# Kernel optimization log

Hardware: AMD Instinct MI355X
Metric: run time of the kernel (lower is better)

## Reference

```python
import jax, jax.numpy as jnp
import numpy as np

N = 50000
E = 800000
DIM = 256
H = 8
HD = DIM // H


def setup_inputs() -> dict:
    key = jax.random.key(0)
    ks = jax.random.split(key, 8)
    s = 0.02
    return {
        "x": jax.random.normal(ks[0], (N, DIM), jnp.float32),
        "src": jax.random.randint(ks[1], (E,), 0, N, jnp.int32),
        "dst": jax.random.randint(ks[2], (E,), 0, N, jnp.int32),
        "Wqkv": jax.random.normal(ks[3], (DIM, 3 * DIM), jnp.float32) * s,
        "bqkv": jnp.zeros((3 * DIM,), jnp.float32),
        "Wout": jax.random.normal(ks[4], (DIM, DIM), jnp.float32) * s,
        "bout": jnp.zeros((DIM,), jnp.float32),
        "W1": jax.random.normal(ks[5], (2 * DIM, DIM), jnpp := jnp.float32) * s,
        "b1": jnp.zeros((DIM,), jnp.float32),
        "W2": jax.random.normal(ks[6], (DIM, DIM), jnp.float32) * s,
        "b2": jnp.zeros((DIM,), jnp.float32),
    }


def reference(x, src, dst, Wqkv, bqkv, Wout, bout, W1, b1, W2, b2):
    n = x.shape[0]
    scale = 1.0 / np.sqrt(HD).astype(np.float32)
    # QKV projection; torch reshapes [N, 3*dim] -> [N, H, 3*hd] then splits per head
    qkv = (x @ Wqkv + bqkv).reshape(n, H, 3 * HD)
    q, k, v = qkv[..., :HD], qkv[..., HD:2 * HD], qkv[..., 2 * HD:]
    # per-edge attention scores: key at src dotted with query at dst -> [E, H]
    scores = jnp.einsum('ehd,ehd->eh', k[src], q[dst]) * scale
    # edge softmax grouped by destination node
    m = jax.ops.segment_max(scores, dst, num_segments=n)  # [N, H]
    p = jnp.exp(scores - m[dst])
    denom = jax.ops.segment_sum(p, dst, num_segments=n)  # [N, H]
    probs = p / denom[dst]
    # weighted scatter-sum aggregation of source values -> [N, H, HD]
    agg = jax.ops.segment_sum(v[src] * probs[..., None], dst, num_segments=n)
    agg = agg.reshape(n, DIM) @ Wout + bout
    # feed-forward over concat([x, aggregated])
    h = jnp.concatenate([x, agg], axis=1)
    h = jax.nn.gelu(h @ W1 + b1, approximate=False)
    return h @ W2 + b2
```

## Files before the change

kernel.cpp:

```cpp
#include <hip/hip_runtime.h>
#include <hip/hip_bf16.h>
#include <math.h>

#define NDIM 256
#define HDIM 32
#define SCB 512

typedef __attribute__((ext_vector_type(8))) short bf16x8;
typedef __attribute__((ext_vector_type(4))) float f32x4;
typedef __attribute__((ext_vector_type(2))) float f32x2;
typedef unsigned long long ull;

__device__ inline float bf2f(unsigned short u) {
  union { unsigned int i; float f; } c; c.i = ((unsigned int)u) << 16; return c.f;
}
__device__ inline unsigned short f2bf(float f) {
  union { float f; unsigned int i; } c; c.f = f;
  unsigned int x = c.i;
  unsigned int lsb = (x >> 16) & 1u;
  x += 0x7fffu + lsb;
  return (unsigned short)(x >> 16);
}
__device__ inline float4 ldbf4(const unsigned short* p) {
  ull raw = *(const ull*)p;
  float4 f;
  f.x = bf2f((unsigned short)(raw));
  f.y = bf2f((unsigned short)(raw >> 16));
  f.z = bf2f((unsigned short)(raw >> 32));
  f.w = bf2f((unsigned short)(raw >> 48));
  return f;
}
__device__ inline void stbf4(unsigned short* p, float4 v) {
  ull raw = (ull)f2bf(v.x) | ((ull)f2bf(v.y) << 16)
          | ((ull)f2bf(v.z) << 32) | ((ull)f2bf(v.w) << 48);
  *(ull*)p = raw;
}
__device__ inline ull pk4_bf16(float v0, float v1, float v2, float v3) {
  return (ull)f2bf(v0) | ((ull)f2bf(v1) << 16) | ((ull)f2bf(v2) << 32) | ((ull)f2bf(v3) << 48);
}

__device__ inline unsigned char f2e4m3(float v) {
#if __has_builtin(__builtin_amdgcn_cvt_pk_fp8_f32)
  return (unsigned char)(__builtin_amdgcn_cvt_pk_fp8_f32(v, v, 0, false) & 0xff);
#else
  union { float f; unsigned int u; } c; c.f = v;
  unsigned char s = (unsigned char)((c.u >> 24) & 0x80);
  float a = fabsf(v);
  if (!(a < 448.f)) return (unsigned char)(s | 0x7e);
  if (a < 0.0009765625f) return s;
  int e = (int)((c.u >> 23) & 0xff) - 127;
  if (e < -6) {
    int q = (int)rintf(ldexpf(a, 9));
    if (q >= 8) return (unsigned char)(s | 0x08);
    return (unsigned char)(s | q);
  }
  int q = (int)rintf(ldexpf(a, 3 - e));
  if (q == 16) { e++; q = 8; }
  if (e > 8) return (unsigned char)(s | 0x7e);
  return (unsigned char)(s | ((e + 7) << 3) | (q - 8));
#endif
}
__device__ inline unsigned int pk4_e4m3(float v0, float v1, float v2, float v3) {
#if __has_builtin(__builtin_amdgcn_cvt_pk_fp8_f32)
  int w = __builtin_amdgcn_cvt_pk_fp8_f32(v0, v1, 0, false);
  w = __builtin_amdgcn_cvt_pk_fp8_f32(v2, v3, w, true);
  return (unsigned int)w;
#else
  return (unsigned int)f2e4m3(v0) | ((unsigned int)f2e4m3(v1) << 8)
       | ((unsigned int)f2e4m3(v2) << 16) | ((unsigned int)f2e4m3(v3) << 24);
#endif
}
template<bool HI>
__device__ inline f32x2 e4m3pk(unsigned int w) {
#if __has_builtin(__builtin_amdgcn_cvt_pk_f32_fp8)
  return __builtin_amdgcn_cvt_pk_f32_fp8((int)w, HI);
#else
  unsigned int h = HI ? (w >> 16) : w;
  f32x2 r;
  #pragma unroll
  for (int j = 0; j < 2; ++j) {
    unsigned char b = (unsigned char)(h >> (8 * j));
    int e = (b >> 3) & 0xf, mm = b & 7;
    float val = e ? ldexpf((float)(8 + mm), e - 10) : ldexpf((float)mm, -9);
    r[j] = (b & 0x80) ? -val : val;
  }
  return r;
#endif
}

__global__ void fuse0_k(
    const float* __restrict__ x, unsigned short* __restrict__ xb, int n8, int nbx,
    const float* __restrict__ Wqkv, unsigned short* __restrict__ wqkvt,
    const float* __restrict__ W1, unsigned short* __restrict__ wf,
    const float* __restrict__ W2, unsigned short* __restrict__ w2t,
    const float* __restrict__ Wout, const float* __restrict__ bout,
    const float* __restrict__ b1, float* __restrict__ bc, int nbw,
    const int* __restrict__ dst, int* __restrict__ deg, int* __restrict__ erank, int E)
{
  int b = blockIdx.x;
  int tid = threadIdx.x;
  if (b < nbx) {
    int i = b * 256 + tid;
    if (i < n8) {
      const float* p = x + (size_t)i * 8;
      float4 a = *(const float4*)p;
      float4 bv = *(const float4*)(p + 4);
      ull lo = (ull)f2bf(a.x) | ((ull)f2bf(a.y) << 16) | ((ull)f2bf(a.z) << 32) | ((ull)f2bf(a.w) << 48);
      ull hi = (ull)f2bf(bv.x) | ((ull)f2bf(bv.y) << 16) | ((ull)f2bf(bv.z) << 32) | ((ull)f2bf(bv.w) << 48);
      ull* d = (ull*)(xb + (size_t)i * 8);
      d[0] = lo; d[1] = hi;
    }
    return;
  }
  b -= nbx;
  if (b < nbw) {
    int idx = b * 256 + tid;
    if (idx < 196608) {
      int j = idx >> 8, k = idx & 255;
      int seg = j >> 8, jj = j & 255;
      int h = jj >> 5, t = jj & 31;
      int orig = h * 96 + seg * 32 + t;
      wqkvt[(size_t)j * 256 + k] = f2bf(Wqkv[(size_t)k * 768 + orig]);
    } else if (idx < 262144) {
      int i2 = idx - 196608;
      int n = i2 >> 8, k = i2 & 255;
      wf[(size_t)n * 512 + k] = f2bf(W1[(size_t)k * 256 + n]);
    } else if (idx < 327680) {
      int i3 = idx - 262144;
      int n = i3 >> 8, k = i3 & 255;
      w2t[(size_t)n * 256 + k] = f2bf(W2[(size_t)k * 256 + n]);
    } else if (idx < 393216) {
      int i4 = idx - 327680;
      int a = i4 >> 8, n = i4 & 255;
      float s = 0.f;
      #pragma unroll 4
      for (int j = 0; j < 256; ++j)
        s += Wout[(size_t)a * 256 + j] * W1[(size_t)(256 + j) * 256 + n];
      wf[(size_t)n * 512 + 256 + a] = f2bf(s);
    } else if (idx < 393472) {
      int n = idx - 393216;
      float s = b1[n];
      for (int j = 0; j < 256; ++j)
        s += bout[j] * W1[(size_t)(256 + j) * 256 + n];
      bc[n] = s;
    }
    return;
  }
  b -= nbw;
  int e = b * 256 + tid;
  if (e < E) {
    int r = atomicAdd(&deg[dst[e]], 1);
    erank[e] = r;
  }
}

__global__ __launch_bounds__(SCB) void bsum_k(const int* __restrict__ deg, int* __restrict__ bsum, int n) {
  int tid = threadIdx.x;
  int i = blockIdx.x * SCB + tid;
  int v = (i < n) ? deg[i] : 0;
  #pragma unroll
  for (int d = 1; d < 64; d <<= 1) v += __shfl_xor(v, d);
  __shared__ int wsum[8];
  if ((tid & 63) == 0) wsum[tid >> 6] = v;
  __syncthreads();
  if (tid == 0) {
    int s = 0;
    #pragma unroll
    for (int j = 0; j < 8; ++j) s += wsum[j];
    bsum[blockIdx.x] = s;
  }
}

__global__ __launch_bounds__(128) void bscan_k(int* __restrict__ bsum, int nb) {
  __shared__ int tmp[128];
  int tid = threadIdx.x;
  int v = (tid < nb) ? bsum[tid] : 0;
  tmp[tid] = v;
  __syncthreads();
  for (int d = 1; d < 128; d <<= 1) {
    int t = (tid >= d) ? tmp[tid - d] : 0;
    __syncthreads();
    tmp[tid] += t;
    __syncthreads();
  }
  if (tid < nb) bsum[tid] = tmp[tid];
}

__global__ __launch_bounds__(SCB) void offs_k(const int* __restrict__ deg, const int* __restrict__ bsum,
                                              int* __restrict__ offs, int n) {
  int tid = threadIdx.x, lane = tid & 63, wid = tid >> 6;
  int b = blockIdx.x;
  int i = b * SCB + tid;
  int v = (i < n) ? deg[i] : 0;
  int incl = v;
  #pragma unroll
  for (int d = 1; d < 64; d <<= 1) { int t = __shfl_up(incl, d); if (lane >= d) incl += t; }
  __shared__ int wsum[8];
  if (lane == 63) wsum[wid] = incl;
  __syncthreads();
  if (tid < 8) {
    int s = wsum[tid];
    #pragma unroll
    for (int d = 1; d < 8; d <<= 1) { int t = __shfl_up(s, d); if (tid >= d) s += t; }
    wsum[tid] = s;
  }
  __syncthreads();
  int base = (b > 0 ? bsum[b - 1] : 0) + (wid > 0 ? wsum[wid - 1] : 0);
  if (i < n) offs[i] = base + incl - v;
  if (i == n - 1) offs[n] = base + incl;
}

__global__ void scatter2_k(const int* __restrict__ src, const int* __restrict__ dstv,
                           const int* __restrict__ offs, const int* __restrict__ erank,
                           int* __restrict__ ssrc, int E) {
  int e = blockIdx.x * 256 + threadIdx.x;
  if (e < E) ssrc[offs[dstv[e]] + erank[e]] = src[e];
}

__global__ __launch_bounds__(256) void attn_k(
    const unsigned short* Q,
    const unsigned char* __restrict__ K8,
    const unsigned char* __restrict__ V8,
    const int* __restrict__ offs,
    const int* __restrict__ ssrc,
    unsigned short* agg, int N)
{
  int n = blockIdx.x * 4 + (threadIdx.x >> 6);
  if (n >= N) return;
  int lane = threadIdx.x & 63;
  int col = lane << 2;
  const float scale = 0.17677669529663689f;
  float4 q4 = ldbf4(Q + (size_t)n * NDIM + col);
  q4.x *= scale; q4.y *= scale; q4.z *= scale; q4.w *= scale;
  int e0 = offs[n], e1 = offs[n + 1];
  float den = 0.f;
  float ax = 0.f, ay = 0.f, az = 0.f, aw = 0.f;
  int e = e0;
  for (; e + 8 <= e1; e += 8) {
    unsigned int kw[8], vw[8];
    #pragma unroll
    for (int j = 0; j < 8; ++j) {
      int s = ssrc[e + j];
      kw[j] = *(const unsigned int*)(K8 + (size_t)s * NDIM + col);
      vw[j] = *(const unsigned int*)(V8 + (size_t)s * NDIM + col);
    }
    float d[8];
    #pragma unroll
    for (int j = 0; j < 8; ++j) {
      f32x2 k01 = e4m3pk<false>(kw[j]);
      f32x2 k23 = e4m3pk<true>(kw[j]);
      d[j] = q4.x * k01[0] + q4.y * k01[1] + q4.z * k23[0] + q4.w * k23[1];
    }
    #pragma unroll
    for (int j = 0; j < 8; ++j) {
      d[j] += __shfl_xor(d[j], 1);
      d[j] += __shfl_xor(d[j], 2);
      d[j] += __shfl_xor(d[j], 4);
    }
    #pragma unroll
    for (int j = 0; j < 8; ++j) {
      float p = __expf(d[j]);
      den += p;
      f32x2 v01 = e4m3pk<false>(vw[j]);
      f32x2 v23 = e4m3pk<true>(vw[j]);
      ax += p * v01[0]; ay += p * v01[1];
      az += p * v23[0]; aw += p * v23[1];
    }
  }
  for (; e + 4 <= e1; e += 4) {
    unsigned int kw[4], vw[4];
    #pragma unroll
    for (int j = 0; j < 4; ++j) {
      int s = ssrc[e + j];
      kw[j] = *(const unsigned int*)(K8 + (size_t)s * NDIM + col);
      vw[j] = *(const unsigned int*)(V8 + (size_t)s * NDIM + col);
    }
    float d[4];
    #pragma unroll
    for (int j = 0; j < 4; ++j) {
      f32x2 k01 = e4m3pk<false>(kw[j]);
      f32x2 k23 = e4m3pk<true>(kw[j]);
      d[j] = q4.x * k01[0] + q4.y * k01[1] + q4.z * k23[0] + q4.w * k23[1];
    }
    #pragma unroll
    for (int j = 0; j < 4; ++j) {
      d[j] += __shfl_xor(d[j], 1);
      d[j] += __shfl_xor(d[j], 2);
      d[j] += __shfl_xor(d[j], 4);
    }
    #pragma unroll
    for (int j = 0; j < 4; ++j) {
      float p = __expf(d[j]);
      den += p;
      f32x2 v01 = e4m3pk<false>(vw[j]);
      f32x2 v23 = e4m3pk<true>(vw[j]);
      ax += p * v01[0]; ay += p * v01[1];
      az += p * v23[0]; aw += p * v23[1];
    }
  }
  for (; e < e1; ++e) {
    int s = ssrc[e];
    unsigned int kw = *(const unsigned int*)(K8 + (size_t)s * NDIM + col);
    unsigned int vw = *(const unsigned int*)(V8 + (size_t)s * NDIM + col);
    f32x2 k01 = e4m3pk<false>(kw);
    f32x2 k23 = e4m3pk<true>(kw);
    float d = q4.x * k01[0] + q4.y * k01[1] + q4.z * k23[0] + q4.w * k23[1];
    d += __shfl_xor(d, 1);
    d += __shfl_xor(d, 2);
    d += __shfl_xor(d, 4);
    float p = __expf(d);
    den += p;
    f32x2 v01 = e4m3pk<false>(vw);
    f32x2 v23 = e4m3pk<true>(vw);
    ax += p * v01[0]; ay += p * v01[1];
    az += p * v23[0]; aw += p * v23[1];
  }
  float inv = (den > 0.f) ? 1.f / den : 0.f;
  stbf4(agg + (size_t)n * NDIM + col, make_float4(ax * inv, ay * inv, az * inv, aw * inv));
}

__global__ __launch_bounds__(256, 4) void qkv_k(
    const unsigned short* __restrict__ A1, const unsigned short* __restrict__ Wt,
    const float* __restrict__ bias,
    unsigned short* __restrict__ Oq, unsigned char* __restrict__ Ok, unsigned char* __restrict__ Ov,
    int M)
{
  __shared__ char smem[32768];
  unsigned short* As = (unsigned short*)smem;
  unsigned short* Bs = (unsigned short*)(smem + 16384);
  const int tid = threadIdx.x;
  const int lane = tid & 63;
  const int wid = tid >> 6;

  const int nwg = gridDim.x;
  const int q8 = nwg >> 3, r8 = nwg & 7;
  const int xcd = blockIdx.x & 7, idx8 = blockIdx.x >> 3;
  const int swz = (xcd < r8 ? xcd * (q8 + 1) : r8 * (q8 + 1) + (xcd - r8) * q8) + idx8;
  const int nct = 6;
  const int bmt = swz / nct;
  const int bnt = swz - bmt * nct;
  const int bm = bmt * 128;
  const int bn = bnt * 128;

  const int wr = (wid >> 1) << 6;
  const int wc = (wid & 1) << 6;
  const int l15 = lane & 15, lhi = lane >> 4;
  const int srow = lane >> 3;
  const int ssl = (((lane & 7) ^ (lane >> 3)) << 3);

  f32x4 acc[4][4];
  #pragma unroll
  for (int i = 0; i < 4; ++i)
    #pragma unroll
    for (int j = 0; j < 4; ++j) acc[i][j] = (f32x4){0.f, 0.f, 0.f, 0.f};

  for (int k0 = 0; k0 < 256; k0 += 64) {
    #pragma unroll
    for (int t = 0; t < 4; ++t) {
      int qi = wid * 4 + t;
      const unsigned short* ga = A1 + (size_t)(bm + qi * 8 + srow) * 256 + k0 + ssl;
      __builtin_amdgcn_global_load_lds(
          (const __attribute__((address_space(1))) void*)ga,
          (__attribute__((address_space(3))) void*)&As[qi * 512], 16, 0, 0);
      const unsigned short* gb = Wt + (size_t)(bn + qi * 8 + srow) * 256 + k0 + ssl;
      __builtin_amdgcn_global_load_lds(
          (const __attribute__((address_space(1))) void*)gb,
          (__attribute__((address_space(3))) void*)&Bs[qi * 512], 16, 0, 0);
    }
    __syncthreads();
    #pragma unroll
    for (int kk = 0; kk < 64; kk += 32) {
      bf16x8 af[4], bfr[4];
      #pragma unroll
      for (int mi = 0; mi < 4; ++mi) {
        int rA = wr + mi * 16 + l15;
        af[mi] = *(const bf16x8*)&As[rA * 64 + ((((kk >> 3) + lhi) ^ (rA & 7)) << 3)];
      }
      #pragma unroll
      for (int ni = 0; ni < 4; ++ni) {
        int rB = wc + ni * 16 + l15;
        bfr[ni] = *(const bf16x8*)&Bs[rB * 64 + ((((kk >> 3) + lhi) ^ (rB & 7)) << 3)];
      }
      #pragma unroll
      for (int mi = 0; mi < 4; ++mi)
        #pragma unroll
        for (int ni = 0; ni < 4; ++ni)
          acc[mi][ni] = __builtin_amdgcn_mfma_f32_16x16x32_bf16(bfr[ni], af[mi], acc[mi][ni], 0, 0, 0);
    }
    __syncthreads();
  }

  const int seg = (bn + wc) >> 8;
  const int jjbase = (bn + wc) & 255;
  char* slabB = smem + wid * 8192;
  if (seg == 0) {
    #pragma unroll
    for (int ni = 0; ni < 4; ++ni) {
      int cl = ni * 16 + (lhi << 2);
      int jj = jjbase + cl;
      float4 bb = *(const float4*)&bias[(jj >> 5) * 96 + (jj & 31)];
      #pragma unroll
      for (int mi = 0; mi < 4; ++mi) {
        int rl = mi * 16 + l15;
        *(ull*)&slabB[rl * 128 + ((cl * 2) ^ ((rl & 7) << 4))] = pk4_bf16(
            acc[mi][ni][0] + bb.x, acc[mi][ni][1] + bb.y,
            acc[mi][ni][2] + bb.z, acc[mi][ni][3] + bb.w);
      }
    }
    asm volatile("s_waitcnt lgkmcnt(0)" ::: "memory");
    __builtin_amdgcn_sched_barrier(0);
    int rl0 = lane >> 3, co = (lane & 7) << 4;
    #pragma unroll
    for (int t = 0; t < 8; ++t) {
      int rl = t * 8 + rl0;
      int gr = bm + wr + rl;
      if (gr < M)
        *(float4*)&Oq[(size_t)gr * NDIM + jjbase + (co >> 1)] =
            *(float4*)&slabB[rl * 128 + (co ^ ((rl & 7) << 4))];
    }
  } else {
    unsigned char* dstp = (seg == 1) ? Ok : Ov;
    #pragma unroll
    for (int ni = 0; ni < 4; ++ni) {
      int cl = ni * 16 + (lhi << 2);
      int jj = jjbase + cl;
      float4 bb = *(const float4*)&bias[(jj >> 5) * 96 + seg * 32 + (jj & 31)];
      #pragma unroll
      for (int mi = 0; mi < 4; ++mi) {
        int rl = mi * 16 + l15;
        *(unsigned int*)&slabB[rl * 64 + (cl ^ ((rl & 3) << 4))] = pk4_e4m3(
            acc[mi][ni][0] + bb.x, acc[mi][ni][1] + bb.y,
            acc[mi][ni][2] + bb.z, acc[mi][ni][3] + bb.w);
      }
    }
    asm volatile("s_waitcnt lgkmcnt(0)" ::: "memory");
    __builtin_amdgcn_sched_barrier(0);
    int rl0 = lane >> 2, co = (lane & 3) << 4;
    #pragma unroll
    for (int t = 0; t < 4; ++t) {
      int rl = t * 16 + rl0;
      int gr = bm + wr + rl;
      if (gr < M)
        *(float4*)&dstp[(size_t)gr * NDIM + jjbase + co] =
            *(float4*)&slabB[rl * 64 + (co ^ ((rl & 3) << 4))];
    }
  }
}

template<int EPI>
__global__ __launch_bounds__(256, 4) void mgemm_k(
    const unsigned short* __restrict__ A1, const unsigned short* __restrict__ A2,
    const unsigned short* __restrict__ Wt, const float* __restrict__ bias,
    float* __restrict__ Cf, unsigned short* __restrict__ Cb,
    int M, int K1, int K, int Ncol, int ldb, int nct)
{
  __shared__ char smem[32768];
  unsigned short* As = (unsigned short*)smem;
  unsigned short* Bs = (unsigned short*)(smem + 16384);
  const int tid = threadIdx.x;
  const int lane = tid & 63;
  const int wid = tid >> 6;

  const int nwg = gridDim.x;
  const int q8 = nwg >> 3, r8 = nwg & 7;
  const int xcd = blockIdx.x & 7, idx8 = blockIdx.x >> 3;
  const int swz = (xcd < r8 ? xcd * (q8 + 1) : r8 * (q8 + 1) + (xcd - r8) * q8) + idx8;
  const int bmt = swz / nct;
  const int bnt = swz - bmt * nct;
  const int bm = bmt * 128;
  const int bn = bnt * 128;

  const int wr = (wid >> 1) << 6;
  const int wc = (wid & 1) << 6;
  const int l15 = lane & 15, lhi = lane >> 4;
  const int srow = lane >> 3;
  const int ssl = (((lane & 7) ^ (lane >> 3)) << 3);

  f32x4 acc[4][4];
  #pragma unroll
  for (int i = 0; i < 4; ++i)
    #pragma unroll
    for (int j = 0; j < 4; ++j) acc[i][j] = (f32x4){0.f, 0.f, 0.f, 0.f};

  for (int k0 = 0; k0 < K; k0 += 64) {
    const unsigned short* Ab;
    int ks;
    if (k0 < K1) { Ab = A1; ks = k0; } else { Ab = A2; ks = k0 - K1; }
    #pragma unroll
    for (int t = 0; t < 4; ++t) {
      int qi = wid * 4 + t;
      const unsigned short* ga = Ab + (size_t)(bm + qi * 8 + srow) * 256 + ks + ssl;
      __builtin_amdgcn_global_load_lds(
          (const __attribute__((address_space(1))) void*)ga,
          (__attribute__((address_space(3))) void*)&As[qi * 512], 16, 0, 0);
      const unsigned short* gb = Wt + (size_t)(bn + qi * 8 + srow) * ldb + k0 + ssl;
      __builtin_amdgcn_global_load_lds(
          (const __attribute__((address_space(1))) void*)gb,
          (__attribute__((address_space(3))) void*)&Bs[qi * 512], 16, 0, 0);
    }
    __syncthreads();
    #pragma unroll
    for (int kk = 0; kk < 64; kk += 32) {
      bf16x8 af[4], bfr[4];
      #pragma unroll
      for (int mi = 0; mi < 4; ++mi) {
        int rA = wr + mi * 16 + l15;
        af[mi] = *(const bf16x8*)&As[rA * 64 + ((((kk >> 3) + lhi) ^ (rA & 7)) << 3)];
      }
      #pragma unroll
      for (int ni = 0; ni < 4; ++ni) {
        int rB = wc + ni * 16 + l15;
        bfr[ni] = *(const bf16x8*)&Bs[rB * 64 + ((((kk >> 3) + lhi) ^ (rB & 7)) << 3)];
      }
      #pragma unroll
      for (int mi = 0; mi < 4; ++mi)
        #pragma unroll
        for (int ni = 0; ni < 4; ++ni)
          acc[mi][ni] = __builtin_amdgcn_mfma_f32_16x16x32_bf16(bfr[ni], af[mi], acc[mi][ni], 0, 0, 0);
    }
    __syncthreads();
  }

  char* slabB = smem + wid * 8192;
  if (EPI == 0) {
    #pragma unroll
    for (int half = 0; half < 2; ++half) {
      #pragma unroll
      for (int nj = 0; nj < 2; ++nj) {
        int ni = half * 2 + nj;
        int cl = nj * 16 + (lhi << 2);
        float4 bb = *(const float4*)&bias[bn + wc + half * 32 + cl];
        #pragma unroll
        for (int mi = 0; mi < 4; ++mi) {
          int rl = mi * 16 + l15;
          *(float4*)&slabB[rl * 128 + ((cl * 4) ^ ((rl & 7) << 4))] = make_float4(
              acc[mi][ni][0] + bb.x, acc[mi][ni][1] + bb.y,
              acc[mi][ni][2] + bb.z, acc[mi][ni][3] + bb.w);
        }
      }
      asm volatile("s_waitcnt lgkmcnt(0)" ::: "memory");
      __builtin_amdgcn_sched_barrier(0);
      int rl0 = lane >> 3, co = (lane & 7) << 4;
      #pragma unroll
      for (int t = 0; t < 8; ++t) {
        int rl = t * 8 + rl0;
        int gr = bm + wr + rl;
        if (gr < M)
          *(float4*)&Cf[(size_t)gr * Ncol + bn + wc + half * 32 + (co >> 2)] =
              *(float4*)&slabB[rl * 128 + (co ^ ((rl & 7) << 4))];
      }
      if (half == 0) {
        asm volatile("s_waitcnt lgkmcnt(0)" ::: "memory");
        __builtin_amdgcn_sched_barrier(0);
      }
    }
  } else {
    #pragma unroll
    for (int ni = 0; ni < 4; ++ni) {
      int cl = ni * 16 + (lhi << 2);
      float4 bb = *(const float4*)&bias[bn + wc + cl];
      #pragma unroll
      for (int mi = 0; mi < 4; ++mi) {
        int rl = mi * 16 + l15;
        float v0 = acc[mi][ni][0] + bb.x;
        float v1 = acc[mi][ni][1] + bb.y;
        float v2 = acc[mi][ni][2] + bb.z;
        float v3 = acc[mi][ni][3] + bb.w;
        v0 = 0.5f * v0 * (1.0f + erff(v0 * 0.70710678118654752f));
        v1 = 0.5f * v1 * (1.0f + erff(v1 * 0.70710678118654752f));
        v2 = 0.5f * v2 * (1.0f + erff(v2 * 0.70710678118654752f));
        v3 = 0.5f * v3 * (1.0f + erff(v3 * 0.70710678118654752f));
        *(ull*)&slabB[rl * 128 + ((cl * 2) ^ ((rl & 7) << 4))] = pk4_bf16(v0, v1, v2, v3);
      }
    }
    asm volatile("s_waitcnt lgkmcnt(0)" ::: "memory");
    __builtin_amdgcn_sched_barrier(0);
    int rl0 = lane >> 3, co = (lane & 7) << 4;
    #pragma unroll
    for (int t = 0; t < 8; ++t) {
      int rl = t * 8 + rl0;
      int gr = bm + wr + rl;
      if (gr < M)
        *(float4*)&Cb[(size_t)gr * Ncol + bn + wc + (co >> 1)] =
            *(float4*)&slabB[rl * 128 + (co ^ ((rl & 7) << 4))];
    }
  }
}

extern "C" void kernel_launch(void* const* d_in, const int* in_sizes, int n_in,
                              void* d_out, int out_size, void* d_ws, size_t ws_size,
                              hipStream_t stream) {
  (void)n_in; (void)out_size; (void)ws_size;
  const float* x    = (const float*)d_in[0];
  const int*   src  = (const int*)d_in[1];
  const int*   dst  = (const int*)d_in[2];
  const float* Wqkv = (const float*)d_in[3];
  const float* bqkv = (const float*)d_in[4];
  const float* Wout = (const float*)d_in[5];
  const float* bout = (const float*)d_in[6];
  const float* W1   = (const float*)d_in[7];
  const float* b1   = (const float*)d_in[8];
  const float* W2   = (const float*)d_in[9];
  const float* b2   = (const float*)d_in[10];
  float* out = (float*)d_out;

  const int N = in_sizes[0] / NDIM;
  const int E = in_sizes[1];
  const int Mp = (N + 127) & ~127;
  const int nb = (N + SCB - 1) / SCB;

  char* ws = (char*)d_ws;
  size_t off = 0;
  auto alloc = [&](size_t bytes) -> char* {
    char* p = ws + off;
    off += (bytes + 255) & ~(size_t)255;
    return p;
  };
  unsigned short* xb   = (unsigned short*)alloc((size_t)Mp * NDIM * 2);
  unsigned short* Q    = (unsigned short*)alloc((size_t)Mp * NDIM * 2);
  unsigned short* Kb   = (unsigned short*)alloc((size_t)Mp * NDIM * 2);
  unsigned short* Vb   = (unsigned short*)alloc((size_t)Mp * NDIM * 2);
  unsigned short* wqkvt = (unsigned short*)alloc((size_t)768 * 256 * 2);
  unsigned short* wft   = (unsigned short*)alloc((size_t)256 * 512 * 2);
  unsigned short* w2t   = (unsigned short*)alloc((size_t)256 * 256 * 2);
  float*          bc    = (float*)alloc(256 * 4);
  int* deg    = (int*)alloc((size_t)N * 4);
  int* offs   = (int*)alloc((size_t)(N + 1) * 4);
  int* erank  = (int*)alloc((size_t)E * 4);
  int* ssrc   = (int*)alloc((size_t)E * 4);
  int* bsum   = (int*)alloc((size_t)nb * 4);

  unsigned char* K8 = (unsigned char*)Kb;
  unsigned char* V8 = (unsigned char*)Vb;
  unsigned short* agg = Q;
  unsigned short* h1  = Kb;

  const int n8  = N * NDIM / 8;
  const int nbx = (n8 + 255) / 256;
  const int nbw = (393472 + 255) / 256;
  const int nsc = (E + 255) / 256;
  const int mt  = Mp / 128;

  hipMemsetAsync(deg, 0, (size_t)N * 4, stream);

  fuse0_k<<<nbx + nbw + nsc, 256, 0, stream>>>(
      x, xb, n8, nbx, Wqkv, wqkvt, W1, wft, W2, w2t, Wout, bout, b1, bc, nbw,
      dst, deg, erank, E);

  bsum_k<<<nb, SCB, 0, stream>>>(deg, bsum, N);
  bscan_k<<<1, 128, 0, stream>>>(bsum, nb);
  offs_k<<<nb, SCB, 0, stream>>>(deg, bsum, offs, N);

  scatter2_k<<<nsc, 256, 0, stream>>>(src, dst, offs, erank, ssrc, E);

  qkv_k<<<mt * 6, 256, 0, stream>>>(xb, wqkvt, bqkv, Q, K8, V8, N);

  attn_k<<<(N + 3) / 4, 256, 0, stream>>>(Q, K8, V8, offs, ssrc, agg, N);

  mgemm_k<2><<<mt * 2, 256, 0, stream>>>(
      xb, agg, wft, bc, nullptr, h1, N, 256, 512, 256, 512, 2);

  mgemm_k<0><<<mt * 2, 256, 0, stream>>>(
      h1, nullptr, w2t, b2, out, nullptr, N, 256, 256, 256, 256, 2);
}
```

Measured before the change: 220.8 us.

## Fuse degree histogram into QKV GEMM launch and replicate counters eightfold

The edge-degree histogram moves out of the prep kernel and into the same launch as the QKV GEMM, so the atomic histogram blocks run alongside the GEMM blocks. Degree counters are replicated eight ways by block index to reduce atomic contention, and the scan kernels combine the replicas and emit per-replica base offsets for the scatter. Edge ranks shrink to 16-bit. The cost is a larger memset, extra reads in the scan kernels, and a rank that could overflow 16 bits on very high-degree nodes.

```diff
diff --git a/kernel.cpp b/kernel.cpp
--- a/kernel.cpp
+++ b/kernel.cpp
@@ -88,14 +88,13 @@
 #endif
 }
 
-__global__ void fuse0_k(
+__global__ void prep_k(
     const float* __restrict__ x, unsigned short* __restrict__ xb, int n8, int nbx,
     const float* __restrict__ Wqkv, unsigned short* __restrict__ wqkvt,
     const float* __restrict__ W1, unsigned short* __restrict__ wf,
     const float* __restrict__ W2, unsigned short* __restrict__ w2t,
     const float* __restrict__ Wout, const float* __restrict__ bout,
-    const float* __restrict__ b1, float* __restrict__ bc, int nbw,
-    const int* __restrict__ dst, int* __restrict__ deg, int* __restrict__ erank, int E)
+    const float* __restrict__ b1, float* __restrict__ bc)
 {
   int b = blockIdx.x;
   int tid = threadIdx.x;
@@ -113,51 +112,187 @@
     return;
   }
   b -= nbx;
-  if (b < nbw) {
-    int idx = b * 256 + tid;
-    if (idx < 196608) {
-      int j = idx >> 8, k = idx & 255;
-      int seg = j >> 8, jj = j & 255;
-      int h = jj >> 5, t = jj & 31;
-      int orig = h * 96 + seg * 32 + t;
-      wqkvt[(size_t)j * 256 + k] = f2bf(Wqkv[(size_t)k * 768 + orig]);
-    } else if (idx < 262144) {
-      int i2 = idx - 196608;
-      int n = i2 >> 8, k = i2 & 255;
-      wf[(size_t)n * 512 + k] = f2bf(W1[(size_t)k * 256 + n]);
-    } else if (idx < 327680) {
-      int i3 = idx - 262144;
-      int n = i3 >> 8, k = i3 & 255;
-      w2t[(size_t)n * 256 + k] = f2bf(W2[(size_t)k * 256 + n]);
-    } else if (idx < 393216) {
-      int i4 = idx - 327680;
-      int a = i4 >> 8, n = i4 & 255;
-      float s = 0.f;
-      #pragma unroll 4
-      for (int j = 0; j < 256; ++j)
-        s += Wout[(size_t)a * 256 + j] * W1[(size_t)(256 + j) * 256 + n];
-      wf[(size_t)n * 512 + 256 + a] = f2bf(s);
-    } else if (idx < 393472) {
-      int n = idx - 393216;
-      float s = b1[n];
-      for (int j = 0; j < 256; ++j)
-        s += bout[j] * W1[(size_t)(256 + j) * 256 + n];
-      bc[n] = s;
+  int idx = b * 256 + tid;
+  if (idx < 196608) {
+    int j = idx >> 8, k = idx & 255;
+    int seg = j >> 8, jj = j & 255;
+    int h = jj >> 5, t = jj & 31;
+    int orig = h * 96 + seg * 32 + t;
+    wqkvt[(size_t)j * 256 + k] = f2bf(Wqkv[(size_t)k * 768 + orig]);
+  } else if (idx < 262144) {
+    int i2 = idx - 196608;
+    int n = i2 >> 8, k = i2 & 255;
+    wf[(size_t)n * 512 + k] = f2bf(W1[(size_t)k * 256 + n]);
+  } else if (idx < 327680) {
+    int i3 = idx - 262144;
+    int n = i3 >> 8, k = i3 & 255;
+    w2t[(size_t)n * 256 + k] = f2bf(W2[(size_t)k * 256 + n]);
+  } else if (idx < 393216) {
+    int i4 = idx - 327680;
+    int a = i4 >> 8, n = i4 & 255;
+    float s = 0.f;
+    #pragma unroll 4
+    for (int j = 0; j < 256; ++j)
+      s += Wout[(size_t)a * 256 + j] * W1[(size_t)(256 + j) * 256 + n];
+    wf[(size_t)n * 512 + 256 + a] = f2bf(s);
+  } else if (idx < 393472) {
+    int n = idx - 393216;
+    float s = b1[n];
+    for (int j = 0; j < 256; ++j)
+      s += bout[j] * W1[(size_t)(256 + j) * 256 + n];
+    bc[n] = s;
+  }
+}
+
+__global__ __launch_bounds__(256, 4) void histqkv_k(
+    const int* __restrict__ dstv, int* __restrict__ deg8,
+    unsigned short* __restrict__ erank, int E, int Nn, int nhist,
+    const unsigned short* __restrict__ A1, const unsigned short* __restrict__ Wt,
+    const float* __restrict__ bias,
+    unsigned short* __restrict__ Oq, unsigned char* __restrict__ Ok, unsigned char* __restrict__ Ov,
+    int M)
+{
+  __shared__ char smem[32768];
+  if (blockIdx.x < nhist) {
+    int b = blockIdx.x;
+    int e = b * 256 + threadIdx.x;
+    if (e < E) {
+      int rep = b & 7;
+      int r = atomicAdd(&deg8[(size_t)rep * Nn + dstv[e]], 1);
+      erank[e] = (unsigned short)r;
     }
     return;
   }
-  b -= nbw;
-  int e = b * 256 + tid;
-  if (e < E) {
-    int r = atomicAdd(&deg[dst[e]], 1);
-    erank[e] = r;
-  }
-}
-
-__global__ __launch_bounds__(SCB) void bsum_k(const int* __restrict__ deg, int* __restrict__ bsum, int n) {
+  unsigned short* As = (unsigned short*)smem;
+  unsigned short* Bs = (unsigned short*)(smem + 16384);
+  const int tid = threadIdx.x;
+  const int lane = tid & 63;
+  const int wid = tid >> 6;
+
+  const int nwg = gridDim.x - nhist;
+  const int bid = blockIdx.x - nhist;
+  const int q8 = nwg >> 3, r8 = nwg & 7;
+  const int xcd = bid & 7, idx8 = bid >> 3;
+  const int swz = (xcd < r8 ? xcd * (q8 + 1) : r8 * (q8 + 1) + (xcd - r8) * q8) + idx8;
+  const int nct = 6;
+  const int bmt = swz / nct;
+  const int bnt = swz - bmt * nct;
+  const int bm = bmt * 128;
+  const int bn = bnt * 128;
+
+  const int wr = (wid >> 1) << 6;
+  const int wc = (wid & 1) << 6;
+  const int l15 = lane & 15, lhi = lane >> 4;
+  const int srow = lane >> 3;
+  const int ssl = (((lane & 7) ^ (lane >> 3)) << 3);
+
+  f32x4 acc[4][4];
+  #pragma unroll
+  for (int i = 0; i < 4; ++i)
+    #pragma unroll
+    for (int j = 0; j < 4; ++j) acc[i][j] = (f32x4){0.f, 0.f, 0.f, 0.f};
+
+  for (int k0 = 0; k0 < 256; k0 += 64) {
+    #pragma unroll
+    for (int t = 0; t < 4; ++t) {
+      int qi = wid * 4 + t;
+      const unsigned short* ga = A1 + (size_t)(bm + qi * 8 + srow) * 256 + k0 + ssl;
+      __builtin_amdgcn_global_load_lds(
+          (const __attribute__((address_space(1))) void*)ga,
+          (__attribute__((address_space(3))) void*)&As[qi * 512], 16, 0, 0);
+      const unsigned short* gb = Wt + (size_t)(bn + qi * 8 + srow) * 256 + k0 + ssl;
+      __builtin_amdgcn_global_load_lds(
+          (const __attribute__((address_space(1))) void*)gb,
+          (__attribute__((address_space(3))) void*)&Bs[qi * 512], 16, 0, 0);
+    }
+    __syncthreads();
+    #pragma unroll
+    for (int kk = 0; kk < 64; kk += 32) {
+      bf16x8 af[4], bfr[4];
+      #pragma unroll
+      for (int mi = 0; mi < 4; ++mi) {
+        int rA = wr + mi * 16 + l15;
+        af[mi] = *(const bf16x8*)&As[rA * 64 + ((((kk >> 3) + lhi) ^ (rA & 7)) << 3)];
+      }
+      #pragma unroll
+      for (int ni = 0; ni < 4; ++ni) {
+        int rB = wc + ni * 16 + l15;
+        bfr[ni] = *(const bf16x8*)&Bs[rB * 64 + ((((kk >> 3) + lhi) ^ (rB & 7)) << 3)];
+      }
+      #pragma unroll
+      for (int mi = 0; mi < 4; ++mi)
+        #pragma unroll
+        for (int ni = 0; ni < 4; ++ni)
+          acc[mi][ni] = __builtin_amdgcn_mfma_f32_16x16x32_bf16(bfr[ni], af[mi], acc[mi][ni], 0, 0, 0);
+    }
+    __syncthreads();
+  }
+
+  const int seg = (bn + wc) >> 8;
+  const int jjbase = (bn + wc) & 255;
+  char* slabB = smem + wid * 8192;
+  if (seg == 0) {
+    #pragma unroll
+    for (int ni = 0; ni < 4; ++ni) {
+      int cl = ni * 16 + (lhi << 2);
+      int jj = jjbase + cl;
+      float4 bb = *(const float4*)&bias[(jj >> 5) * 96 + (jj & 31)];
+      #pragma unroll
+      for (int mi = 0; mi < 4; ++mi) {
+        int rl = mi * 16 + l15;
+        *(ull*)&slabB[rl * 128 + ((cl * 2) ^ ((rl & 7) << 4))] = pk4_bf16(
+            acc[mi][ni][0] + bb.x, acc[mi][ni][1] + bb.y,
+            acc[mi][ni][2] + bb.z, acc[mi][ni][3] + bb.w);
+      }
+    }
+    asm volatile("s_waitcnt lgkmcnt(0)" ::: "memory");
+    __builtin_amdgcn_sched_barrier(0);
+    int rl0 = lane >> 3, co = (lane & 7) << 4;
+    #pragma unroll
+    for (int t = 0; t < 8; ++t) {
+      int rl = t * 8 + rl0;
+      int gr = bm + wr + rl;
+      if (gr < M)
+        *(float4*)&Oq[(size_t)gr * NDIM + jjbase + (co >> 1)] =
+            *(float4*)&slabB[rl * 128 + (co ^ ((rl & 7) << 4))];
+    }
+  } else {
+    unsigned char* dstp = (seg == 1) ? Ok : Ov;
+    #pragma unroll
+    for (int ni = 0; ni < 4; ++ni) {
+      int cl = ni * 16 + (lhi << 2);
+      int jj = jjbase + cl;
+      float4 bb = *(const float4*)&bias[(jj >> 5) * 96 + seg * 32 + (jj & 31)];
+      #pragma unroll
+      for (int mi = 0; mi < 4; ++mi) {
+        int rl = mi * 16 + l15;
+        *(unsigned int*)&slabB[rl * 64 + (cl ^ ((rl & 3) << 4))] = pk4_e4m3(
+            acc[mi][ni][0] + bb.x, acc[mi][ni][1] + bb.y,
+            acc[mi][ni][2] + bb.z, acc[mi][ni][3] + bb.w);
+      }
+    }
+    asm volatile("s_waitcnt lgkmcnt(0)" ::: "memory");
+    __builtin_amdgcn_sched_barrier(0);
+    int rl0 = lane >> 2, co = (lane & 3) << 4;
+    #pragma unroll
+    for (int t = 0; t < 4; ++t) {
+      int rl = t * 16 + rl0;
+      int gr = bm + wr + rl;
+      if (gr < M)
+        *(float4*)&dstp[(size_t)gr * NDIM + jjbase + co] =
+            *(float4*)&slabB[rl * 64 + (co ^ ((rl & 3) << 4))];
+    }
+  }
+}
+
+__global__ __launch_bounds__(SCB) void bsum_k(const int* __restrict__ deg8, int* __restrict__ bsum, int n) {
   int tid = threadIdx.x;
   int i = blockIdx.x * SCB + tid;
-  int v = (i < n) ? deg[i] : 0;
+  int v = 0;
+  if (i < n) {
+    #pragma unroll
+    for (int r = 0; r < 8; ++r) v += deg8[(size_t)r * n + i];
+  }
   #pragma unroll
   for (int d = 1; d < 64; d <<= 1) v += __shfl_xor(v, d);
   __shared__ int wsum[8];
@@ -186,12 +321,20 @@
   if (tid < nb) bsum[tid] = tmp[tid];
 }
 
-__global__ __launch_bounds__(SCB) void offs_k(const int* __restrict__ deg, const int* __restrict__ bsum,
-                                              int* __restrict__ offs, int n) {
+__global__ __launch_bounds__(SCB) void offs_k(const int* __restrict__ deg8, const int* __restrict__ bsum,
+                                              int* __restrict__ offs, int* __restrict__ rbase, int n) {
   int tid = threadIdx.x, lane = tid & 63, wid = tid >> 6;
   int b = blockIdx.x;
   int i = b * SCB + tid;
-  int v = (i < n) ? deg[i] : 0;
+  int c[8];
+  int v = 0;
+  if (i < n) {
+    #pragma unroll
+    for (int r = 0; r < 8; ++r) { c[r] = deg8[(size_t)r * n + i]; v += c[r]; }
+  } else {
+    #pragma unroll
+    for (int r = 0; r < 8; ++r) c[r] = 0;
+  }
   int incl = v;
   #pragma unroll
   for (int d = 1; d < 64; d <<= 1) { int t = __shfl_up(incl, d); if (lane >= d) incl += t; }
@@ -206,15 +349,24 @@
   }
   __syncthreads();
   int base = (b > 0 ? bsum[b - 1] : 0) + (wid > 0 ? wsum[wid - 1] : 0);
-  if (i < n) offs[i] = base + incl - v;
+  if (i < n) {
+    int start = base + incl - v;
+    offs[i] = start;
+    int p = start;
+    #pragma unroll
+    for (int r = 0; r < 8; ++r) { rbase[(size_t)r * n + i] = p; p += c[r]; }
+  }
   if (i == n - 1) offs[n] = base + incl;
 }
 
 __global__ void scatter2_k(const int* __restrict__ src, const int* __restrict__ dstv,
-                           const int* __restrict__ offs, const int* __restrict__ erank,
-                           int* __restrict__ ssrc, int E) {
+                           const int* __restrict__ rbase, const unsigned short* __restrict__ erank,
+                           int* __restrict__ ssrc, int E, int Nn) {
   int e = blockIdx.x * 256 + threadIdx.x;
-  if (e < E) ssrc[offs[dstv[e]] + erank[e]] = src[e];
+  if (e < E) {
+    int rep = (e >> 8) & 7;
+    ssrc[rbase[(size_t)rep * Nn + dstv[e]] + erank[e]] = src[e];
+  }
 }
 
 __global__ __launch_bounds__(256) void attn_k(
@@ -319,134 +471,6 @@
   stbf4(agg + (size_t)n * NDIM + col, make_float4(ax * inv, ay * inv, az * inv, aw * inv));
 }
 
-__global__ __launch_bounds__(256, 4) void qkv_k(
-    const unsigned short* __restrict__ A1, const unsigned short* __restrict__ Wt,
-    const float* __restrict__ bias,
-    unsigned short* __restrict__ Oq, unsigned char* __restrict__ Ok, unsigned char* __restrict__ Ov,
-    int M)
-{
-  __shared__ char smem[32768];
-  unsigned short* As = (unsigned short*)smem;
-  unsigned short* Bs = (unsigned short*)(smem + 16384);
-  const int tid = threadIdx.x;
-  const int lane = tid & 63;
-  const int wid = tid >> 6;
-
-  const int nwg = gridDim.x;
-  const int q8 = nwg >> 3, r8 = nwg & 7;
-  const int xcd = blockIdx.x & 7, idx8 = blockIdx.x >> 3;
-  const int swz = (xcd < r8 ? xcd * (q8 + 1) : r8 * (q8 + 1) + (xcd - r8) * q8) + idx8;
-  const int nct = 6;
-  const int bmt = swz / nct;
-  const int bnt = swz - bmt * nct;
-  const int bm = bmt * 128;
-  const int bn = bnt * 128;
-
-  const int wr = (wid >> 1) << 6;
-  const int wc = (wid & 1) << 6;
-  const int l15 = lane & 15, lhi = lane >> 4;
-  const int srow = lane >> 3;
-  const int ssl = (((lane & 7) ^ (lane >> 3)) << 3);
-
-  f32x4 acc[4][4];
-  #pragma unroll
-  for (int i = 0; i < 4; ++i)
-    #pragma unroll
-    for (int j = 0; j < 4; ++j) acc[i][j] = (f32x4){0.f, 0.f, 0.f, 0.f};
-
-  for (int k0 = 0; k0 < 256; k0 += 64) {
-    #pragma unroll
-    for (int t = 0; t < 4; ++t) {
-      int qi = wid * 4 + t;
-      const unsigned short* ga = A1 + (size_t)(bm + qi * 8 + srow) * 256 + k0 + ssl;
-      __builtin_amdgcn_global_load_lds(
-          (const __attribute__((address_space(1))) void*)ga,
-          (__attribute__((address_space(3))) void*)&As[qi * 512], 16, 0, 0);
-      const unsigned short* gb = Wt + (size_t)(bn + qi * 8 + srow) * 256 + k0 + ssl;
-      __builtin_amdgcn_global_load_lds(
-          (const __attribute__((address_space(1))) void*)gb,
-          (__attribute__((address_space(3))) void*)&Bs[qi * 512], 16, 0, 0);
-    }
-    __syncthreads();
-    #pragma unroll
-    for (int kk = 0; kk < 64; kk += 32) {
-      bf16x8 af[4], bfr[4];
-      #pragma unroll
-      for (int mi = 0; mi < 4; ++mi) {
-        int rA = wr + mi * 16 + l15;
-        af[mi] = *(const bf16x8*)&As[rA * 64 + ((((kk >> 3) + lhi) ^ (rA & 7)) << 3)];
-      }
-      #pragma unroll
-      for (int ni = 0; ni < 4; ++ni) {
-        int rB = wc + ni * 16 + l15;
-        bfr[ni] = *(const bf16x8*)&Bs[rB * 64 + ((((kk >> 3) + lhi) ^ (rB & 7)) << 3)];
-      }
-      #pragma unroll
-      for (int mi = 0; mi < 4; ++mi)
-        #pragma unroll
-        for (int ni = 0; ni < 4; ++ni)
-          acc[mi][ni] = __builtin_amdgcn_mfma_f32_16x16x32_bf16(bfr[ni], af[mi], acc[mi][ni], 0, 0, 0);
-    }
-    __syncthreads();
-  }
-
-  const int seg = (bn + wc) >> 8;
-  const int jjbase = (bn + wc) & 255;
-  char* slabB = smem + wid * 8192;
-  if (seg == 0) {
-    #pragma unroll
-    for (int ni = 0; ni < 4; ++ni) {
-      int cl = ni * 16 + (lhi << 2);
-      int jj = jjbase + cl;
-      float4 bb = *(const float4*)&bias[(jj >> 5) * 96 + (jj & 31)];
-      #pragma unroll
-      for (int mi = 0; mi < 4; ++mi) {
-        int rl = mi * 16 + l15;
-        *(ull*)&slabB[rl * 128 + ((cl * 2) ^ ((rl & 7) << 4))] = pk4_bf16(
-            acc[mi][ni][0] + bb.x, acc[mi][ni][1] + bb.y,
-            acc[mi][ni][2] + bb.z, acc[mi][ni][3] + bb.w);
-      }
-    }
-    asm volatile("s_waitcnt lgkmcnt(0)" ::: "memory");
-    __builtin_amdgcn_sched_barrier(0);
-    int rl0 = lane >> 3, co = (lane & 7) << 4;
-    #pragma unroll
-    for (int t = 0; t < 8; ++t) {
-      int rl = t * 8 + rl0;
-      int gr = bm + wr + rl;
-      if (gr < M)
-        *(float4*)&Oq[(size_t)gr * NDIM + jjbase + (co >> 1)] =
-            *(float4*)&slabB[rl * 128 + (co ^ ((rl & 7) << 4))];
-    }
-  } else {
-    unsigned char* dstp = (seg == 1) ? Ok : Ov;
-    #pragma unroll
-    for (int ni = 0; ni < 4; ++ni) {
-      int cl = ni * 16 + (lhi << 2);
-      int jj = jjbase + cl;
-      float4 bb = *(const float4*)&bias[(jj >> 5) * 96 + seg * 32 + (jj & 31)];
-      #pragma unroll
-      for (int mi = 0; mi < 4; ++mi) {
-        int rl = mi * 16 + l15;
-        *(unsigned int*)&slabB[rl * 64 + (cl ^ ((rl & 3) << 4))] = pk4_e4m3(
-            acc[mi][ni][0] + bb.x, acc[mi][ni][1] + bb.y,
-            acc[mi][ni][2] + bb.z, acc[mi][ni][3] + bb.w);
-      }
-    }
-    asm volatile("s_waitcnt lgkmcnt(0)" ::: "memory");
-    __builtin_amdgcn_sched_barrier(0);
-    int rl0 = lane >> 2, co = (lane & 3) << 4;
-    #pragma unroll
-    for (int t = 0; t < 4; ++t) {
-      int rl = t * 16 + rl0;
-      int gr = bm + wr + rl;
-      if (gr < M)
-        *(float4*)&dstp[(size_t)gr * NDIM + jjbase + co] =
-            *(float4*)&slabB[rl * 64 + (co ^ ((rl & 3) << 4))];
-    }
-  }
-}
-
 template<int EPI>
 __global__ __launch_bounds__(256, 4) void mgemm_k(
     const unsigned short* __restrict__ A1, const unsigned short* __restrict__ A2,
@@ -624,9 +648,10 @@
   unsigned short* wft   = (unsigned short*)alloc((size_t)256 * 512 * 2);
   unsigned short* w2t   = (unsigned short*)alloc((size_t)256 * 256 * 2);
   float*          bc    = (float*)alloc(256 * 4);
-  int* deg    = (int*)alloc((size_t)N * 4);
+  int* deg8   = (int*)alloc((size_t)8 * N * 4);
+  int* rbase  = (int*)alloc((size_t)8 * N * 4);
   int* offs   = (int*)alloc((size_t)(N + 1) * 4);
-  int* erank  = (int*)alloc((size_t)E * 4);
+  unsigned short* erank = (unsigned short*)alloc((size_t)E * 2);
   int* ssrc   = (int*)alloc((size_t)E * 4);
   int* bsum   = (int*)alloc((size_t)nb * 4);
 
@@ -641,19 +666,20 @@
   const int nsc = (E + 255) / 256;
   const int mt  = Mp / 128;
 
-  hipMemsetAsync(deg, 0, (size_t)N * 4, stream);
-
-  fuse0_k<<<nbx + nbw + nsc, 256, 0, stream>>>(
-      x, xb, n8, nbx, Wqkv, wqkvt, W1, wft, W2, w2t, Wout, bout, b1, bc, nbw,
-      dst, deg, erank, E);
-
-  bsum_k<<<nb, SCB, 0, stream>>>(deg, bsum, N);
+  hipMemsetAsync(deg8, 0, (size_t)8 * N * 4, stream);
+
+  prep_k<<<nbx + nbw, 256, 0, stream>>>(
+      x, xb, n8, nbx, Wqkv, wqkvt, W1, wft, W2, w2t, Wout, bout, b1, bc);
+
+  histqkv_k<<<nsc + mt * 6, 256, 0, stream>>>(
+      dst, deg8, erank, E, N, nsc,
+      xb, wqkvt, bqkv, Q, K8, V8, N);
+
+  bsum_k<<<nb, SCB, 0, stream>>>(deg8, bsum, N);
   bscan_k<<<1, 128, 0, stream>>>(bsum, nb);
-  offs_k<<<nb, SCB, 0, stream>>>(deg, bsum, offs, N);
-
-  scatter2_k<<<nsc, 256, 0, stream>>>(src, dst, offs, erank, ssrc, E);
-
-  qkv_k<<<mt * 6, 256, 0, stream>>>(xb, wqkvt, bqkv, Q, K8, V8, N);
+  offs_k<<<nb, SCB, 0, stream>>>(deg8, bsum, offs, rbase, N);
+
+  scatter2_k<<<nsc, 256, 0, stream>>>(src, dst, rbase, erank, ssrc, E, N);
 
   attn_k<<<(N + 3) / 4, 256, 0, stream>>>(Q, K8, V8, offs, ssrc, agg, N);
 
```

Result: no change. 221.2 us (median of 3 runs) (+0.2%).
